# Kernel optimization log

Hardware: AMD Instinct MI355X
Metric: run time of the kernel (lower is better)

The kernel has to match this reference:

```python
import jax, jax.numpy as jnp
import numpy as np

N, E, G = 50000, 1600000, 64
N_SPECIES, D_ATTR, D, N_RBF = 16, 16, 32, 8
CUTOFF = 5.0
SCALE, SHIFT = 1.0, 0.0


def setup_inputs() -> dict:
    key = jax.random.key(0)
    ks = jax.random.split(key, 20)

    def w(k, shape):
        fan_in = shape[-2] if len(shape) > 1 else shape[-1]
        return jax.random.normal(k, shape, dtype=jnp.float32) / np.sqrt(fan_in)

    return {
        "x": jax.random.randint(ks[0], (N, 1), 0, N_SPECIES),
        "pos": 3.0 * jax.random.normal(ks[1], (N, 3), dtype=jnp.float32),
        "edge_index": jax.random.randint(ks[2], (2, E), 0, N),
        "period_vec": 0.1 * jax.random.normal(ks[3], (E, 3), dtype=jnp.float32),
        "batch": jnp.sort(jax.random.randint(ks[4], (N,), 0, G)),
        "W_elem": w(ks[5], (N_SPECIES, D_ATTR)),
        "W0": w(ks[6], (D_ATTR, D)),
        "b0": jnp.zeros((D,), jnp.float32),
        "Wr1": w(ks[7], (3, N_RBF, D)),
        "br1": jnp.zeros((3, D), jnp.float32),
        "Wr2": w(ks[8], (3, D, D)),
        "Wmsg": w(ks[9], (3, D, D)),
        "Wattr": w(ks[10], (3, D_ATTR, D)),
        "Wself": w(ks[11], (3, D, D)),
        "bconv": jnp.zeros((3, D), jnp.float32),
        "wsh": w(ks[12], (3, 4)),
        "Wp1": w(ks[13], (D, 16)),
        "bp1": jnp.zeros((16,), jnp.float32),
        "Wp2": w(ks[14], (16, 1)),
        "bp2": jnp.zeros((1,), jnp.float32),
    }


def reference(x, pos, edge_index, period_vec, batch, W_elem, W0, b0, Wr1, br1,
              Wr2, Wmsg, Wattr, Wself, bconv, wsh, Wp1, bp1, Wp2, bp2):
    src, dst = edge_index[0], edge_index[1]

    # node_attr_layer: species embedding (gather), then first_atom_embed linear
    x_attr = W_elem[x[:, 0]]                              # [N, D_ATTR]
    h = x_attr @ W0 + b0                                  # [N, D]

    # edge_attr_layer: PBC edge vectors, lengths, l<=1 spherical harmonics
    edge_vec = pos[dst] - pos[src] + period_vec           # [E, 3]
    edge_len = jnp.linalg.norm(edge_vec, axis=-1, keepdims=True)  # [E, 1]
    unit = edge_vec / (edge_len + 1e-9)
    edge_sh = jnp.concatenate([jnp.ones_like(edge_len), unit], axis=-1)  # [E, 4]

    # edge_embedding_layer: Gaussian radial basis of edge lengths
    centers = jnp.linspace(0.0, CUTOFF, N_RBF, dtype=pos.dtype)
    gamma = jnp.asarray((N_RBF / CUTOFF) ** 2, pos.dtype)
    rbf = jnp.exp(-gamma * (edge_len - centers) ** 2)     # [E, N_RBF]

    # 3 conv layers: gather -> per-edge transform -> scatter-sum -> node update
    for i in range(3):
        rw = jax.nn.relu(rbf @ Wr1[i] + br1[i]) @ Wr2[i]  # [E, D] radial MLP
        sh_w = edge_sh @ wsh[i]                           # [E] sh mixing
        msg = (h[src] @ Wmsg[i]) * rw * sh_w[:, None]     # [E, D]
        agg = jax.ops.segment_sum(msg, dst, num_segments=N)  # [N, D]
        h = jax.nn.silu(agg + x_attr @ Wattr[i] + h @ Wself[i] + bconv[i])

    # post_conv layers
    h = jax.nn.silu(h @ Wp1 + bp1)                        # [N, 16]
    h = (h @ Wp2 + bp2)[:, 0]                             # [N] (squeeze)

    # scatter-sum pooling over graphs + affine energy scaling
    e = jax.ops.segment_sum(h, batch, num_segments=G)     # [G]
    return (e * SCALE + SHIFT)[:, None]                   # [G, 1]
```

## Files before the change

kernel.cpp:

```cpp
#include <hip/hip_runtime.h>
#include <hip/hip_fp16.h>
#include <math.h>

constexpr int N_NODES  = 50000;
constexpr int N_EDGES  = 1600000;
constexpr int G_GRAPHS = 64;
constexpr int D        = 32;
constexpr int D_ATTR   = 16;
constexpr int N_RBF    = 8;

constexpr int   TBL      = 8192;
constexpr int   TBL_ROWS = TBL + 1;
constexpr float LMAX     = 10.0f;

constexpr int BUCKET = 80;

__device__ __forceinline__ float silu(float x) {
    return x / (1.0f + __expf(-x));
}

__global__ void node_init_kernel(const int* __restrict__ x,
                                 const float* __restrict__ W_elem,
                                 const float* __restrict__ W0,
                                 const float* __restrict__ b0,
                                 const float* __restrict__ Wmsg0,
                                 float* __restrict__ x_attr,
                                 float* __restrict__ h,
                                 __half* __restrict__ hm,
                                 int* __restrict__ cursor) {
    int t = blockIdx.x * blockDim.x + threadIdx.x;
    int n = t >> 5, c = t & 31;
    if (n >= N_NODES) return;
    int sp = x[n];
    const float* we = W_elem + sp * D_ATTR;
    float acc = b0[c];
#pragma unroll
    for (int a = 0; a < D_ATTR; ++a) acc += we[a] * W0[a * D + c];
    h[n * D + c] = acc;
    if (c < D_ATTR) x_attr[n * D_ATTR + c] = we[c];
    if (c == 0) cursor[n] = n * BUCKET;
    float m = 0.0f;
#pragma unroll
    for (int j = 0; j < D; ++j) {
        float hj = __shfl(acc, j, 32);
        m = fmaf(hj, Wmsg0[j * D + c], m);
    }
    hm[n * D + c] = __float2half(m);
}

__global__ void scatter_kernel(const int* __restrict__ eidx,
                               const float* __restrict__ pos,
                               const float* __restrict__ period,
                               const float* __restrict__ wsh,
                               int* __restrict__ cursor,
                               float4* __restrict__ rec) {
    int e = blockIdx.x * blockDim.x + threadIdx.x;
    if (e >= N_EDGES) return;
    int s = eidx[e];
    int d = eidx[N_EDGES + e];
    float vx = pos[d * 3 + 0] - pos[s * 3 + 0] + period[e * 3 + 0];
    float vy = pos[d * 3 + 1] - pos[s * 3 + 1] + period[e * 3 + 1];
    float vz = pos[d * 3 + 2] - pos[s * 3 + 2] + period[e * 3 + 2];
    float len = sqrtf(vx * vx + vy * vy + vz * vz);
    float inv = 1.0f / (len + 1e-9f);
    int idx = (int)fminf(len * ((float)TBL / LMAX) + 0.5f, (float)TBL);
    float sw[3];
#pragma unroll
    for (int l = 0; l < 3; ++l)
        sw[l] = wsh[l * 4 + 0] + (vx * wsh[l * 4 + 1] + vy * wsh[l * 4 + 2] + vz * wsh[l * 4 + 3]) * inv;
    int k = atomicAdd(&cursor[d], 1);
    if (k < d * BUCKET + BUCKET)
        rec[k] = make_float4(__int_as_float(s | (idx << 16)), sw[0], sw[1], sw[2]);
}

__global__ void table_kernel(const float* __restrict__ Wr1,
                             const float* __restrict__ br1,
                             const float* __restrict__ Wr2,
                             __half* __restrict__ table) {
    int t = blockIdx.x * blockDim.x + threadIdx.x;
    if (t >= 3 * TBL_ROWS) return;
    int l = t / TBL_ROWS;
    int idx = t % TBL_ROWS;
    float len = (float)idx * (LMAX / (float)TBL);
    const float gamma = (8.0f / 5.0f) * (8.0f / 5.0f);
    float rbf[N_RBF];
#pragma unroll
    for (int k = 0; k < N_RBF; ++k) {
        float dd = len - (float)k * (5.0f / 7.0f);
        rbf[k] = __expf(-gamma * dd * dd);
    }
    float out[D];
#pragma unroll
    for (int c = 0; c < D; ++c) out[c] = 0.0f;
    for (int j = 0; j < D; ++j) {
        float z = br1[l * D + j];
#pragma unroll
        for (int k = 0; k < N_RBF; ++k) z += rbf[k] * Wr1[l * N_RBF * D + k * D + j];
        z = fmaxf(z, 0.0f);
        const float* w2 = Wr2 + l * D * D + j * D;
#pragma unroll
        for (int c = 0; c < D; ++c) out[c] += z * w2[c];
    }
    __half* dst = table + ((size_t)(l * TBL_ROWS + idx)) * D;
#pragma unroll
    for (int c = 0; c < D; ++c) dst[c] = __float2half(out[c]);
}

template <int LAYER, bool WRITE_HM>
__global__ void conv_kernel(const __half* __restrict__ hm,
                            const float4* __restrict__ rec,
                            const int* __restrict__ cursor,
                            const float* __restrict__ x_attr,
                            const __half* __restrict__ table,
                            const float* __restrict__ Wattr,
                            const float* __restrict__ Wself,
                            const float* __restrict__ bconv,
                            const float* __restrict__ Wmsg_next,
                            float* __restrict__ h,
                            __half* __restrict__ hm_next) {
    int gtid = blockIdx.x * blockDim.x + threadIdx.x;
    int node = gtid >> 6;
    if (node >= N_NODES) return;
    int lane = threadIdx.x & 63;
    int qw = lane >> 4;
    int q  = lane & 15;

    const __half2* tab2 = (const __half2*)(table + ((size_t)LAYER * TBL_ROWS) * D);
    const __half2* hm2  = (const __half2*)hm;
    int beg = node * BUCKET;
    int end = cursor[node];
    if (end > beg + BUCKET) end = beg + BUCKET;

    float ax0 = 0.f, ay0 = 0.f, ax1 = 0.f, ay1 = 0.f;
    float ax2 = 0.f, ay2 = 0.f, ax3 = 0.f, ay3 = 0.f;
    int k = beg + qw;
    for (; k + 12 < end; k += 16) {
        float4 r0 = rec[k];
        float4 r1 = rec[k + 4];
        float4 r2 = rec[k + 8];
        float4 r3 = rec[k + 12];
        int p0 = __float_as_int(r0.x), p1 = __float_as_int(r1.x);
        int p2 = __float_as_int(r2.x), p3 = __float_as_int(r3.x);
        int s0 = p0 & 0xFFFF, s1 = p1 & 0xFFFF, s2 = p2 & 0xFFFF, s3 = p3 & 0xFFFF;
        int i0 = (unsigned)p0 >> 16, i1 = (unsigned)p1 >> 16;
        int i2 = (unsigned)p2 >> 16, i3 = (unsigned)p3 >> 16;
        __half2 t0 = tab2[i0 * 16 + q];
        __half2 t1 = tab2[i1 * 16 + q];
        __half2 t2 = tab2[i2 * 16 + q];
        __half2 t3 = tab2[i3 * 16 + q];
        __half2 m0 = hm2[s0 * 16 + q];
        __half2 m1 = hm2[s1 * 16 + q];
        __half2 m2 = hm2[s2 * 16 + q];
        __half2 m3 = hm2[s3 * 16 + q];
        float sw0 = (LAYER == 0) ? r0.y : (LAYER == 1) ? r0.z : r0.w;
        float sw1 = (LAYER == 0) ? r1.y : (LAYER == 1) ? r1.z : r1.w;
        float sw2 = (LAYER == 0) ? r2.y : (LAYER == 1) ? r2.z : r2.w;
        float sw3 = (LAYER == 0) ? r3.y : (LAYER == 1) ? r3.z : r3.w;
        float2 tf0 = __half22float2(t0), mf0 = __half22float2(m0);
        float2 tf1 = __half22float2(t1), mf1 = __half22float2(m1);
        float2 tf2 = __half22float2(t2), mf2 = __half22float2(m2);
        float2 tf3 = __half22float2(t3), mf3 = __half22float2(m3);
        ax0 = fmaf(tf0.x * mf0.x, sw0, ax0);
        ay0 = fmaf(tf0.y * mf0.y, sw0, ay0);
        ax1 = fmaf(tf1.x * mf1.x, sw1, ax1);
        ay1 = fmaf(tf1.y * mf1.y, sw1, ay1);
        ax2 = fmaf(tf2.x * mf2.x, sw2, ax2);
        ay2 = fmaf(tf2.y * mf2.y, sw2, ay2);
        ax3 = fmaf(tf3.x * mf3.x, sw3, ax3);
        ay3 = fmaf(tf3.y * mf3.y, sw3, ay3);
    }
    for (; k < end; k += 4) {
        float4 r = rec[k];
        int p = __float_as_int(r.x);
        int s = p & 0xFFFF, i = (unsigned)p >> 16;
        float sw = (LAYER == 0) ? r.y : (LAYER == 1) ? r.z : r.w;
        float2 tf = __half22float2(tab2[i * 16 + q]);
        float2 mf = __half22float2(hm2[s * 16 + q]);
        ax0 = fmaf(tf.x * mf.x, sw, ax0);
        ay0 = fmaf(tf.y * mf.y, sw, ay0);
    }
    float ax = (ax0 + ax1) + (ax2 + ax3);
    float ay = (ay0 + ay1) + (ay2 + ay3);
    ax += __shfl_xor(ax, 16);
    ax += __shfl_xor(ax, 32);
    ay += __shfl_xor(ay, 16);
    ay += __shfl_xor(ay, 32);

    int c = lane & 31;
    float vx = __shfl(ax, c >> 1);
    float vy = __shfl(ay, c >> 1);
    float agg = (c & 1) ? vy : vx;

    if ((lane >> 5) == 0) {
        float hload = h[node * D + c];
        float xload = (c < D_ATTR) ? x_attr[node * D_ATTR + c] : 0.0f;
        float pre = agg + bconv[LAYER * D + c];
        const float* Ws = Wself + LAYER * D * D;
        const float* Wa = Wattr + LAYER * D_ATTR * D;
#pragma unroll
        for (int j = 0; j < D; ++j) pre = fmaf(__shfl(hload, j), Ws[j * D + c], pre);
#pragma unroll
        for (int j = 0; j < D_ATTR; ++j) pre = fmaf(__shfl(xload, j), Wa[j * D + c], pre);
        float hn = silu(pre);
        h[node * D + c] = hn;
        if (WRITE_HM) {
            float m = 0.0f;
#pragma unroll
            for (int j = 0; j < D; ++j) m = fmaf(__shfl(hn, j), Wmsg_next[j * D + c], m);
            hm_next[node * D + c] = __float2half(m);
        }
    }
}

__global__ void readout_kernel(const float* __restrict__ h,
                               const int* __restrict__ batch,
                               const float* __restrict__ Wp1,
                               const float* __restrict__ bp1,
                               const float* __restrict__ Wp2,
                               const float* __restrict__ bp2,
                               float* __restrict__ out) {
    int n = blockIdx.x * blockDim.x + threadIdx.x;
    float s = 0.0f;
    int b = -1;
    if (n < N_NODES) {
        b = batch[n];
        const float* hrow = h + n * D;
        float acc2 = bp2[0];
#pragma unroll
        for (int m = 0; m < 16; ++m) {
            float a = bp1[m];
#pragma unroll
            for (int j = 0; j < D; ++j) a += hrow[j] * Wp1[j * 16 + m];
            acc2 += silu(a) * Wp2[m];
        }
        s = acc2;
    }
    unsigned long long valid = __ballot(n < N_NODES);
    if (valid == 0ull) return;
    int firstLane = __ffsll(valid) - 1;
    int b0v = __shfl(b, firstLane);
    bool ok = (b == b0v) || (n >= N_NODES);
    if (__all(ok)) {
#pragma unroll
        for (int o = 32; o > 0; o >>= 1) s += __shfl_down(s, o);
        if ((threadIdx.x & 63) == 0) atomicAdd(out + b0v, s);
    } else {
        if (n < N_NODES) atomicAdd(out + b, s);
    }
}

extern "C" void kernel_launch(void* const* d_in, const int* in_sizes, int n_in,
                              void* d_out, int out_size, void* d_ws, size_t ws_size,
                              hipStream_t stream) {
    const int*   x      = (const int*)d_in[0];
    const float* pos    = (const float*)d_in[1];
    const int*   eidx   = (const int*)d_in[2];
    const float* period = (const float*)d_in[3];
    const int*   batch  = (const int*)d_in[4];
    const float* W_elem = (const float*)d_in[5];
    const float* W0     = (const float*)d_in[6];
    const float* b0     = (const float*)d_in[7];
    const float* Wr1    = (const float*)d_in[8];
    const float* br1    = (const float*)d_in[9];
    const float* Wr2    = (const float*)d_in[10];
    const float* Wmsg   = (const float*)d_in[11];
    const float* Wattr  = (const float*)d_in[12];
    const float* Wself  = (const float*)d_in[13];
    const float* bconv  = (const float*)d_in[14];
    const float* wsh    = (const float*)d_in[15];
    const float* Wp1    = (const float*)d_in[16];
    const float* bp1    = (const float*)d_in[17];
    const float* Wp2    = (const float*)d_in[18];
    const float* bp2    = (const float*)d_in[19];

    char* base = (char*)d_ws;
    size_t off = 0;
    auto carve = [&](size_t bytes) -> void* {
        void* p = base + off;
        off = (off + bytes + 255) & ~(size_t)255;
        return p;
    };
    float*  x_attr = (float*)carve((size_t)N_NODES * D_ATTR * 4);
    float*  h      = (float*)carve((size_t)N_NODES * D * 4);
    __half* hm_a   = (__half*)carve((size_t)N_NODES * D * 2);
    __half* hm_b   = (__half*)carve((size_t)N_NODES * D * 2);
    float4* rec    = (float4*)carve((size_t)N_NODES * BUCKET * 16);
    int*    cursor = (int*)carve((size_t)N_NODES * 4);
    __half* table  = (__half*)carve((size_t)3 * TBL_ROWS * D * 2);
    (void)ws_size; (void)in_sizes; (void)n_in; (void)out_size;

    hipMemsetAsync(d_out, 0, (size_t)G_GRAPHS * 4, stream);

    node_init_kernel<<<(N_NODES * 32 + 255) / 256, 256, 0, stream>>>(
        x, W_elem, W0, b0, Wmsg + 0 * D * D, x_attr, h, hm_a, cursor);
    scatter_kernel<<<(N_EDGES + 255) / 256, 256, 0, stream>>>(eidx, pos, period, wsh, cursor, rec);
    table_kernel<<<(3 * TBL_ROWS + 127) / 128, 128, 0, stream>>>(Wr1, br1, Wr2, table);

    int cgrid = (N_NODES * 64 + 255) / 256;
    conv_kernel<0, true><<<cgrid, 256, 0, stream>>>(
        hm_a, rec, cursor, x_attr, table, Wattr, Wself, bconv, Wmsg + 1 * D * D, h, hm_b);
    conv_kernel<1, true><<<cgrid, 256, 0, stream>>>(
        hm_b, rec, cursor, x_attr, table, Wattr, Wself, bconv, Wmsg + 2 * D * D, h, hm_a);
    conv_kernel<2, false><<<cgrid, 256, 0, stream>>>(
        hm_a, rec, cursor, x_attr, table, Wattr, Wself, bconv, nullptr, h, nullptr);

    readout_kernel<<<(N_NODES + 255) / 256, 256, 0, stream>>>(h, batch, Wp1, bp1, Wp2, bp2,
                                                              (float*)d_out);
}
```

Baseline: 417.7 us.

## Store edge records in edge order and bucket only edge indices

The scatter kernel now writes each edge's packed record coalesced into an edge-ordered staging array and puts only a 4-byte edge index into each destination bucket, instead of a scattered 16-byte record. The conv kernels gain one extra level of indirection: they read the index, then gather the 16-byte record at random, then gather table and hm rows. The edge loop is also reshaped into an 8-way unrolled loop with clamped slots and zero weights for the tail. The aim is to make the scatter writes cheaper, at the cost of random record gathers repeated in all three conv layers.

```diff
diff --git a/kernel.cpp b/kernel.cpp
--- a/kernel.cpp
+++ b/kernel.cpp
@@ -53,7 +53,8 @@
                                const float* __restrict__ period,
                                const float* __restrict__ wsh,
                                int* __restrict__ cursor,
-                               float4* __restrict__ rec) {
+                               float4* __restrict__ staged,
+                               unsigned int* __restrict__ invbuf) {
     int e = blockIdx.x * blockDim.x + threadIdx.x;
     if (e >= N_EDGES) return;
     int s = eidx[e];
@@ -68,9 +69,10 @@
 #pragma unroll
     for (int l = 0; l < 3; ++l)
         sw[l] = wsh[l * 4 + 0] + (vx * wsh[l * 4 + 1] + vy * wsh[l * 4 + 2] + vz * wsh[l * 4 + 3]) * inv;
+    staged[e] = make_float4(__int_as_float(s | (idx << 16)), sw[0], sw[1], sw[2]);
     int k = atomicAdd(&cursor[d], 1);
     if (k < d * BUCKET + BUCKET)
-        rec[k] = make_float4(__int_as_float(s | (idx << 16)), sw[0], sw[1], sw[2]);
+        invbuf[k] = (unsigned int)e;
 }
 
 __global__ void table_kernel(const float* __restrict__ Wr1,
@@ -108,7 +110,8 @@
 
 template <int LAYER, bool WRITE_HM>
 __global__ void conv_kernel(const __half* __restrict__ hm,
-                            const float4* __restrict__ rec,
+                            const float4* __restrict__ staged,
+                            const unsigned int* __restrict__ invbuf,
                             const int* __restrict__ cursor,
                             const float* __restrict__ x_attr,
                             const __half* __restrict__ table,
@@ -131,56 +134,34 @@
     int end = cursor[node];
     if (end > beg + BUCKET) end = beg + BUCKET;
 
-    float ax0 = 0.f, ay0 = 0.f, ax1 = 0.f, ay1 = 0.f;
-    float ax2 = 0.f, ay2 = 0.f, ax3 = 0.f, ay3 = 0.f;
-    int k = beg + qw;
-    for (; k + 12 < end; k += 16) {
-        float4 r0 = rec[k];
-        float4 r1 = rec[k + 4];
-        float4 r2 = rec[k + 8];
-        float4 r3 = rec[k + 12];
-        int p0 = __float_as_int(r0.x), p1 = __float_as_int(r1.x);
-        int p2 = __float_as_int(r2.x), p3 = __float_as_int(r3.x);
-        int s0 = p0 & 0xFFFF, s1 = p1 & 0xFFFF, s2 = p2 & 0xFFFF, s3 = p3 & 0xFFFF;
-        int i0 = (unsigned)p0 >> 16, i1 = (unsigned)p1 >> 16;
-        int i2 = (unsigned)p2 >> 16, i3 = (unsigned)p3 >> 16;
-        __half2 t0 = tab2[i0 * 16 + q];
-        __half2 t1 = tab2[i1 * 16 + q];
-        __half2 t2 = tab2[i2 * 16 + q];
-        __half2 t3 = tab2[i3 * 16 + q];
-        __half2 m0 = hm2[s0 * 16 + q];
-        __half2 m1 = hm2[s1 * 16 + q];
-        __half2 m2 = hm2[s2 * 16 + q];
-        __half2 m3 = hm2[s3 * 16 + q];
-        float sw0 = (LAYER == 0) ? r0.y : (LAYER == 1) ? r0.z : r0.w;
-        float sw1 = (LAYER == 0) ? r1.y : (LAYER == 1) ? r1.z : r1.w;
-        float sw2 = (LAYER == 0) ? r2.y : (LAYER == 1) ? r2.z : r2.w;
-        float sw3 = (LAYER == 0) ? r3.y : (LAYER == 1) ? r3.z : r3.w;
-        float2 tf0 = __half22float2(t0), mf0 = __half22float2(m0);
-        float2 tf1 = __half22float2(t1), mf1 = __half22float2(m1);
-        float2 tf2 = __half22float2(t2), mf2 = __half22float2(m2);
-        float2 tf3 = __half22float2(t3), mf3 = __half22float2(m3);
-        ax0 = fmaf(tf0.x * mf0.x, sw0, ax0);
-        ay0 = fmaf(tf0.y * mf0.y, sw0, ay0);
-        ax1 = fmaf(tf1.x * mf1.x, sw1, ax1);
-        ay1 = fmaf(tf1.y * mf1.y, sw1, ay1);
-        ax2 = fmaf(tf2.x * mf2.x, sw2, ax2);
-        ay2 = fmaf(tf2.y * mf2.y, sw2, ay2);
-        ax3 = fmaf(tf3.x * mf3.x, sw3, ax3);
-        ay3 = fmaf(tf3.y * mf3.y, sw3, ay3);
-    }
-    for (; k < end; k += 4) {
-        float4 r = rec[k];
-        int p = __float_as_int(r.x);
-        int s = p & 0xFFFF, i = (unsigned)p >> 16;
-        float sw = (LAYER == 0) ? r.y : (LAYER == 1) ? r.z : r.w;
-        float2 tf = __half22float2(tab2[i * 16 + q]);
-        float2 mf = __half22float2(hm2[s * 16 + q]);
-        ax0 = fmaf(tf.x * mf.x, sw, ax0);
-        ay0 = fmaf(tf.y * mf.y, sw, ay0);
-    }
-    float ax = (ax0 + ax1) + (ax2 + ax3);
-    float ay = (ay0 + ay1) + (ay2 + ay3);
+    float ax = 0.0f, ay = 0.0f;
+    if (end > beg) {
+        int last = end - 1;
+        for (int base = beg + qw; base < end; base += 32) {
+            unsigned int iv[8];
+#pragma unroll
+            for (int j = 0; j < 8; ++j) {
+                int slot = base + 4 * j;
+                iv[j] = invbuf[slot <= last ? slot : last];
+            }
+            float4 r[8];
+#pragma unroll
+            for (int j = 0; j < 8; ++j) r[j] = staged[iv[j]];
+#pragma unroll
+            for (int j = 0; j < 8; ++j) {
+                int slot = base + 4 * j;
+                int p = __float_as_int(r[j].x);
+                int s = p & 0xFFFF;
+                int i = (unsigned)p >> 16;
+                float sw = (LAYER == 0) ? r[j].y : (LAYER == 1) ? r[j].z : r[j].w;
+                sw = (slot <= last) ? sw : 0.0f;
+                float2 tf = __half22float2(tab2[i * 16 + q]);
+                float2 mf = __half22float2(hm2[s * 16 + q]);
+                ax = fmaf(tf.x * mf.x, sw, ax);
+                ay = fmaf(tf.y * mf.y, sw, ay);
+            }
+        }
+    }
     ax += __shfl_xor(ax, 16);
     ax += __shfl_xor(ax, 32);
     ay += __shfl_xor(ay, 16);
@@ -280,29 +261,31 @@
         off = (off + bytes + 255) & ~(size_t)255;
         return p;
     };
-    float*  x_attr = (float*)carve((size_t)N_NODES * D_ATTR * 4);
-    float*  h      = (float*)carve((size_t)N_NODES * D * 4);
-    __half* hm_a   = (__half*)carve((size_t)N_NODES * D * 2);
-    __half* hm_b   = (__half*)carve((size_t)N_NODES * D * 2);
-    float4* rec    = (float4*)carve((size_t)N_NODES * BUCKET * 16);
-    int*    cursor = (int*)carve((size_t)N_NODES * 4);
-    __half* table  = (__half*)carve((size_t)3 * TBL_ROWS * D * 2);
+    float*        x_attr = (float*)carve((size_t)N_NODES * D_ATTR * 4);
+    float*        h      = (float*)carve((size_t)N_NODES * D * 4);
+    __half*       hm_a   = (__half*)carve((size_t)N_NODES * D * 2);
+    __half*       hm_b   = (__half*)carve((size_t)N_NODES * D * 2);
+    float4*       staged = (float4*)carve((size_t)N_EDGES * 16);
+    unsigned int* invbuf = (unsigned int*)carve((size_t)N_NODES * BUCKET * 4);
+    int*          cursor = (int*)carve((size_t)N_NODES * 4);
+    __half*       table  = (__half*)carve((size_t)3 * TBL_ROWS * D * 2);
     (void)ws_size; (void)in_sizes; (void)n_in; (void)out_size;
 
     hipMemsetAsync(d_out, 0, (size_t)G_GRAPHS * 4, stream);
 
     node_init_kernel<<<(N_NODES * 32 + 255) / 256, 256, 0, stream>>>(
         x, W_elem, W0, b0, Wmsg + 0 * D * D, x_attr, h, hm_a, cursor);
-    scatter_kernel<<<(N_EDGES + 255) / 256, 256, 0, stream>>>(eidx, pos, period, wsh, cursor, rec);
+    scatter_kernel<<<(N_EDGES + 255) / 256, 256, 0, stream>>>(eidx, pos, period, wsh, cursor,
+                                                              staged, invbuf);
     table_kernel<<<(3 * TBL_ROWS + 127) / 128, 128, 0, stream>>>(Wr1, br1, Wr2, table);
 
     int cgrid = (N_NODES * 64 + 255) / 256;
     conv_kernel<0, true><<<cgrid, 256, 0, stream>>>(
-        hm_a, rec, cursor, x_attr, table, Wattr, Wself, bconv, Wmsg + 1 * D * D, h, hm_b);
+        hm_a, staged, invbuf, cursor, x_attr, table, Wattr, Wself, bconv, Wmsg + 1 * D * D, h, hm_b);
     conv_kernel<1, true><<<cgrid, 256, 0, stream>>>(
-        hm_b, rec, cursor, x_attr, table, Wattr, Wself, bconv, Wmsg + 2 * D * D, h, hm_a);
+        hm_b, staged, invbuf, cursor, x_attr, table, Wattr, Wself, bconv, Wmsg + 2 * D * D, h, hm_a);
     conv_kernel<2, false><<<cgrid, 256, 0, stream>>>(
-        hm_a, rec, cursor, x_attr, table, Wattr, Wself, bconv, nullptr, h, nullptr);
+        hm_a, staged, invbuf, cursor, x_attr, table, Wattr, Wself, bconv, nullptr, h, nullptr);
 
     readout_kernel<<<(N_NODES + 255) / 256, 256, 0, stream>>>(h, batch, Wp1, bp1, Wp2, bp2,
                                                               (float*)d_out);
```

New measurement: 439.0 us. 5.1% more time.
